# Kernel tuning notes

Measured on AMD Instinct MI355X. Metric: run time of the kernel, lower is better.

## Reference

```python
import jax, jax.numpy as jnp
import numpy as np

B, S, D = 2, 1024, 1024
L, E, F = 2, 8, 2048


def setup_inputs() -> dict:
    key = jax.random.key(0)
    kx, kp, k1, k2 = jax.random.split(key, 4)
    x = jax.random.normal(kx, (B, S, D), dtype=jnp.float32)
    # prototypes scaled so dot products are O(1), keeping softmax well-behaved
    protos = jax.random.normal(kp, (L, E, D), dtype=jnp.float32) / np.sqrt(D)
    W1 = jax.random.normal(k1, (L, E, D, F), dtype=jnp.float32) * 0.02
    W2 = jax.random.normal(k2, (L, E, F, D), dtype=jnp.float32) * 0.02
    return {"x": x, "protos": protos, "W1": W1, "W2": W2, "k": 2}


def _route(x, protos_l, k):
    # expert_mapping: abs(dot(prototype, input)) per expert, keep top-k, rest -> -inf, softmax
    scores = jnp.abs(jnp.einsum("bsd,ed->bse", x, protos_l))  # [B,S,E]
    topv, _ = jax.lax.top_k(scores, k)
    thresh = topv[..., -1:]  # k-th largest per token
    masked = jnp.where(scores >= thresh, scores, -jnp.inf)
    return jax.nn.softmax(masked, axis=-1)  # [B,S,E]


def reference(x, protos, W1, W2, k):
    n_layers = protos.shape[0]
    for l in range(n_layers):  # fixed small layer loop
        w = _route(x, protos[l], k)  # [B,S,E]
        h = jax.nn.relu(jnp.einsum("bsd,edf->bsef", x, W1[l]))  # [B,S,E,F]
        y = jnp.einsum("bsef,efd,bse->bsd", h, W2[l], w)  # weighted expert mix
        x = x + y
    return x
```

## Files before the change

kernel.cpp:

```cpp
#include <hip/hip_runtime.h>
#include <hip/hip_bf16.h>
#include <cstdint>

#define T_TOKENS 2048
#define DDIM 1024
#define FDIM 2048
#define NEXP 8
#define NLAYER 2
#define BMPAD 64
#define RMAX 4608

#define ATILE_EL 2048
#define BTILE_EL 4096

typedef unsigned short u16;
typedef short bf16x8 __attribute__((ext_vector_type(8)));
typedef u16 u16x8 __attribute__((ext_vector_type(8)));
typedef u16 u16x4v __attribute__((ext_vector_type(4)));
typedef float f32x4 __attribute__((ext_vector_type(4)));

__device__ __forceinline__ u16 bf16_rn(float f) {
  unsigned u = __builtin_bit_cast(unsigned, f);
  u += 0x7fffu + ((u >> 16) & 1u);
  return (u16)(u >> 16);
}
__device__ __forceinline__ float bf16_f(u16 h) {
  unsigned u = ((unsigned)h) << 16;
  return __builtin_bit_cast(float, u);
}

__device__ __forceinline__ void gl16(const void* g, void* l) {
  __builtin_amdgcn_global_load_lds((const __attribute__((address_space(1))) void*)g,
                                   (__attribute__((address_space(3))) void*)l, 16, 0, 0);
}

__global__ __launch_bounds__(256) void route_kernel(
    const float* __restrict__ x, const float* __restrict__ protos,
    int* __restrict__ eid, float* __restrict__ wgt) {
  const int t = blockIdx.x;
  const int tid = threadIdx.x;
  const float* xr = x + (size_t)t * DDIM;
  __shared__ float red[NEXP][256];
  float acc[NEXP];
#pragma unroll
  for (int e = 0; e < NEXP; ++e) acc[e] = 0.f;
  for (int d = tid; d < DDIM; d += 256) {
    float xv = xr[d];
#pragma unroll
    for (int e = 0; e < NEXP; ++e) acc[e] += xv * protos[e * DDIM + d];
  }
#pragma unroll
  for (int e = 0; e < NEXP; ++e) red[e][tid] = acc[e];
  __syncthreads();
  for (int s = 128; s > 0; s >>= 1) {
    if (tid < s) {
#pragma unroll
      for (int e = 0; e < NEXP; ++e) red[e][tid] += red[e][tid + s];
    }
    __syncthreads();
  }
  if (tid == 0) {
    float m1 = -1.f, m2 = -1.f;
    int i1 = 0, i2 = 0;
#pragma unroll
    for (int e = 0; e < NEXP; ++e) {
      float s = fabsf(red[e][0]);
      if (s > m1) { m2 = m1; i2 = i1; m1 = s; i1 = e; }
      else if (s > m2) { m2 = s; i2 = e; }
    }
    float e2 = __expf(m2 - m1);
    float z = 1.f + e2;
    eid[t * 2] = i1;
    eid[t * 2 + 1] = i2;
    wgt[t * 2] = 1.f / z;
    wgt[t * 2 + 1] = e2 / z;
  }
}

__global__ __launch_bounds__(256) void compact_kernel(
    const int* __restrict__ eid, int* __restrict__ cnt, int* __restrict__ offp,
    int* __restrict__ row2token, int* __restrict__ pos) {
  __shared__ int lcnt[NEXP][256];
  __shared__ int s_off[NEXP], s_tot[NEXP];
  const int tid = threadIdx.x;
  const int base = tid * 16;

  int my[16];
#pragma unroll
  for (int i = 0; i < 4; ++i)
    *(int4*)&my[i * 4] = *(const int4*)(eid + base + i * 4);

#pragma unroll
  for (int e = 0; e < NEXP; ++e) {
    int c = 0;
#pragma unroll
    for (int i = 0; i < 16; ++i) c += (my[i] == e) ? 1 : 0;
    lcnt[e][tid] = c;
  }

  for (int r = tid; r < RMAX; r += 256) row2token[r] = -1;
  __syncthreads();

  if (tid < NEXP) {
    int run = 0;
    for (int i = 0; i < 256; ++i) {
      int v = lcnt[tid][i];
      lcnt[tid][i] = run;
      run += v;
    }
    s_tot[tid] = run;
  }
  __syncthreads();
  if (tid == 0) {
    int o = 0;
    for (int e = 0; e < NEXP; ++e) {
      s_off[e] = o;
      o += (s_tot[e] + BMPAD - 1) & ~(BMPAD - 1);
    }
  }
  __syncthreads();

  int myoff[NEXP];
#pragma unroll
  for (int e = 0; e < NEXP; ++e) myoff[e] = s_off[e] + lcnt[e][tid];
#pragma unroll
  for (int i = 0; i < 16; ++i) {
    int r = 0;
#pragma unroll
    for (int e = 0; e < NEXP; ++e) r = (my[i] == e) ? myoff[e] : r;
    row2token[r] = (base + i) >> 1;
    pos[base + i] = r;
#pragma unroll
    for (int e = 0; e < NEXP; ++e) myoff[e] += (my[i] == e) ? 1 : 0;
  }

  if (tid < NEXP) {
    cnt[tid] = s_tot[tid];
    offp[tid] = s_off[tid];
  }
}

__global__ __launch_bounds__(256) void gather_kernel(
    const float* __restrict__ x, const int* __restrict__ row2token,
    u16* __restrict__ Ahi, u16* __restrict__ Alo) {
  const int r = blockIdx.x;
  const int t = row2token[r];
  const int c = threadIdx.x * 4;
  float4 v = make_float4(0.f, 0.f, 0.f, 0.f);
  if (t >= 0) v = *(const float4*)(x + (size_t)t * DDIM + c);
  float vv[4] = {v.x, v.y, v.z, v.w};
  u16x4v hi, lo;
#pragma unroll
  for (int i = 0; i < 4; ++i) {
    u16 h = bf16_rn(vv[i]);
    hi[i] = h;
    lo[i] = bf16_rn(vv[i] - bf16_f(h));
  }
  const size_t el = ((size_t)(r >> 6) * (DDIM >> 5) + (c >> 5)) * ATILE_EL +
                    (size_t)(((c >> 3) & 3) * 64 + (r & 63)) * 8 + (c & 7);
  *(u16x4v*)(Ahi + el) = hi;
  *(u16x4v*)(Alo + el) = lo;
}

template <bool LO>
__global__ __launch_bounds__(256) void wconv_kernel(
    const float* __restrict__ W, u16* __restrict__ Hi, u16* __restrict__ Lo,
    int K, int N) {
  const int e = blockIdx.z, nb = blockIdx.x, kb = blockIdx.y;
  const float* Wp = W + ((size_t)e * K + (size_t)kb * 32) * N + nb * 128;
  __shared__ float tile[32][129];
  const int t = threadIdx.x;
#pragma unroll
  for (int i = 0; i < 4; ++i) {
    const int f4 = i * 256 + t;
    const int kr = f4 >> 5;
    const int c4 = (f4 & 31) * 4;
    float4 v = *(const float4*)(Wp + (size_t)kr * N + c4);
    *(float4*)&tile[kr][c4] = v;
  }
  __syncthreads();
  const size_t tb = (((size_t)e * (N >> 7) + nb) * (K >> 5) + kb) * BTILE_EL;
#pragma unroll
  for (int j = 0; j < 2; ++j) {
    const int cid = j * 256 + t;
    const int n = cid & 127, ksel = cid >> 7;
    u16x8 hv, lv;
#pragma unroll
    for (int i = 0; i < 8; ++i) {
      float f = tile[ksel * 8 + i][n];
      u16 h = bf16_rn(f);
      hv[i] = h;
      if (LO) lv[i] = bf16_rn(f - bf16_f(h));
    }
    *(u16x8*)(Hi + tb + (size_t)cid * 8) = hv;
    if (LO) *(u16x8*)(Lo + tb + (size_t)cid * 8) = lv;
  }
}

template <bool RELU, bool SPLIT, int OUTMODE>
__global__ __launch_bounds__(256, SPLIT ? 3 : 4) void gemm_mfma(
    const u16* __restrict__ Ahi, const u16* __restrict__ Alo,
    const u16* __restrict__ Bhi, const u16* __restrict__ Blo,
    u16* __restrict__ OutHi, u16* __restrict__ OutLo, float* __restrict__ OutF,
    const int* __restrict__ cnt, const int* __restrict__ offp, int K, int N) {
  const int e = blockIdx.z;
  const int cp = (cnt[e] + 63) & ~63;
  if ((int)(blockIdx.y * 64) >= cp) return;
  const int row0 = offp[e] + blockIdx.y * 64;
  const int n0 = blockIdx.x * 128;
  const int nkb = K >> 5;

  constexpr int BUF_EL = SPLIT ? 12288 : 6144;
  __shared__ u16 lds[2 * BUF_EL];

  const int tid = threadIdx.x;
  const int lane = tid & 63;
  const int wid = tid >> 6;
  const int wr = wid >> 1, wc = wid & 1;
  const int lr = lane & 15, kg = lane >> 4;
  const int lo16 = lane << 4;

  f32x4 acc[2][4];
#pragma unroll
  for (int i = 0; i < 2; ++i)
#pragma unroll
    for (int j = 0; j < 4; ++j)
#pragma unroll
      for (int r = 0; r < 4; ++r) acc[i][j][r] = 0.f;

  const size_t abase = (size_t)(row0 >> 6) * nkb * ATILE_EL;
  const size_t bbase = ((size_t)e * (N >> 7) + (n0 >> 7)) * nkb * BTILE_EL;

  auto STAGE = [&](int kb, int b) {
    char* d = (char*)(lds + b * BUF_EL);
    const char* gah = (const char*)(Ahi + abase + (size_t)kb * ATILE_EL);
    const char* gbh = (const char*)(Bhi + bbase + (size_t)kb * BTILE_EL);
    if constexpr (SPLIT) {
      const char* gal = (const char*)(Alo + abase + (size_t)kb * ATILE_EL);
      const char* gbl = (const char*)(Blo + bbase + (size_t)kb * BTILE_EL);
      if (wid == 0) {
#pragma unroll
        for (int i = 0; i < 4; ++i) gl16(gah + i * 1024 + lo16, d + i * 1024);
#pragma unroll
        for (int i = 0; i < 4; ++i) gl16(gal + i * 1024 + lo16, d + 4096 + i * 1024);
      } else if (wid == 1) {
#pragma unroll
        for (int i = 0; i < 8; ++i) gl16(gbh + i * 1024 + lo16, d + 8192 + i * 1024);
      } else if (wid == 2) {
#pragma unroll
        for (int i = 0; i < 8; ++i) gl16(gbl + i * 1024 + lo16, d + 16384 + i * 1024);
      }
    } else {
      if (wid == 0) {
#pragma unroll
        for (int i = 0; i < 4; ++i) gl16(gah + i * 1024 + lo16, d + i * 1024);
      } else if (wid == 1) {
#pragma unroll
        for (int i = 0; i < 4; ++i) gl16(gbh + i * 1024 + lo16, d + 4096 + i * 1024);
      } else if (wid == 2) {
#pragma unroll
        for (int i = 0; i < 4; ++i) gl16(gbh + 4096 + i * 1024 + lo16, d + 8192 + i * 1024);
      }
    }
  };

  STAGE(0, 0);
  __syncthreads();

  int cur = 0;
  for (int kb = 0; kb < nkb; ++kb) {
    if (kb + 1 < nkb) STAGE(kb + 1, cur ^ 1);

    const u16* buf = lds + cur * BUF_EL;
    const u16* AsH = buf;
    const u16* BsH = buf + (SPLIT ? 4096 : 2048);
    bf16x8 ah0 = *(const bf16x8*)&AsH[(kg * 64 + wr * 32 + lr) * 8];
    bf16x8 ah1 = *(const bf16x8*)&AsH[(kg * 64 + wr * 32 + 16 + lr) * 8];
    bf16x8 bh[4];
#pragma unroll
    for (int j = 0; j < 4; ++j)
      bh[j] = *(const bf16x8*)&BsH[(kg * 128 + wc * 64 + j * 16 + lr) * 8];
#pragma unroll
    for (int j = 0; j < 4; ++j) {
      acc[0][j] = __builtin_amdgcn_mfma_f32_16x16x32_bf16(ah0, bh[j], acc[0][j], 0, 0, 0);
      acc[1][j] = __builtin_amdgcn_mfma_f32_16x16x32_bf16(ah1, bh[j], acc[1][j], 0, 0, 0);
    }
    if constexpr (SPLIT) {
      const u16* AsL = buf + 2048;
      const u16* BsL = buf + 8192;
      bf16x8 al0 = *(const bf16x8*)&AsL[(kg * 64 + wr * 32 + lr) * 8];
      bf16x8 al1 = *(const bf16x8*)&AsL[(kg * 64 + wr * 32 + 16 + lr) * 8];
#pragma unroll
      for (int j = 0; j < 4; ++j) {
        bf16x8 bl = *(const bf16x8*)&BsL[(kg * 128 + wc * 64 + j * 16 + lr) * 8];
        acc[0][j] = __builtin_amdgcn_mfma_f32_16x16x32_bf16(ah0, bl, acc[0][j], 0, 0, 0);
        acc[1][j] = __builtin_amdgcn_mfma_f32_16x16x32_bf16(ah1, bl, acc[1][j], 0, 0, 0);
        acc[0][j] = __builtin_amdgcn_mfma_f32_16x16x32_bf16(al0, bh[j], acc[0][j], 0, 0, 0);
        acc[1][j] = __builtin_amdgcn_mfma_f32_16x16x32_bf16(al1, bh[j], acc[1][j], 0, 0, 0);
      }
    }
    __syncthreads();
    cur ^= 1;
  }

  const int nkbO = N >> 5;
#pragma unroll
  for (int i = 0; i < 2; ++i) {
#pragma unroll
    for (int j = 0; j < 4; ++j) {
      const int Cj = n0 + wc * 64 + j * 16 + lr;
      f32x4 v = acc[i][j];
#pragma unroll
      for (int r = 0; r < 4; ++r) {
        const int R = row0 + wr * 32 + i * 16 + kg * 4 + r;
        float f = v[r];
        if (RELU) f = fmaxf(f, 0.f);
        if constexpr (OUTMODE == 0) {
          OutF[(size_t)R * N + Cj] = f;
        } else {
          const size_t el = ((size_t)(R >> 6) * nkbO + (Cj >> 5)) * ATILE_EL +
                            (size_t)(((Cj >> 3) & 3) * 64 + (R & 63)) * 8 + (Cj & 7);
          u16 h = bf16_rn(f);
          OutHi[el] = h;
          if constexpr (OUTMODE == 1) OutLo[el] = bf16_rn(f - bf16_f(h));
        }
      }
    }
  }
}

__global__ __launch_bounds__(256) void apply_kernel(
    const float* __restrict__ ytmp, const int* __restrict__ pos,
    const float* __restrict__ wgt, float* __restrict__ x) {
  const int t = blockIdx.x;
  const int c = threadIdx.x * 4;
  const int p0 = pos[t * 2], p1 = pos[t * 2 + 1];
  const float w0 = wgt[t * 2], w1 = wgt[t * 2 + 1];
  float4 xa = *(float4*)(x + (size_t)t * DDIM + c);
  const float4 y0 = *(const float4*)(ytmp + (size_t)p0 * DDIM + c);
  const float4 y1 = *(const float4*)(ytmp + (size_t)p1 * DDIM + c);
  xa.x += w0 * y0.x + w1 * y1.x;
  xa.y += w0 * y0.y + w1 * y1.y;
  xa.z += w0 * y0.z + w1 * y1.z;
  xa.w += w0 * y0.w + w1 * y1.w;
  *(float4*)(x + (size_t)t * DDIM + c) = xa;
}

extern "C" void kernel_launch(void* const* d_in, const int* in_sizes, int n_in,
                              void* d_out, int out_size, void* d_ws, size_t ws_size,
                              hipStream_t stream) {
  const float* x = (const float*)d_in[0];
  const float* protos = (const float*)d_in[1];
  const float* W1 = (const float*)d_in[2];
  const float* W2 = (const float*)d_in[3];
  float* xcur = (float*)d_out;

  u16* W_hi = (u16*)d_ws;
  u16* W_lo = W_hi + (size_t)NEXP * DDIM * FDIM;
  u16* Ag_hi = W_lo + (size_t)NEXP * DDIM * FDIM;
  u16* Ag_lo = Ag_hi + (size_t)RMAX * DDIM;
  u16* h_hi = Ag_lo + (size_t)RMAX * DDIM;
  u16* h_lo = h_hi + (size_t)RMAX * FDIM;
  float* ytmp = (float*)(h_lo + (size_t)RMAX * FDIM);
  float* wgt = ytmp + (size_t)RMAX * DDIM;
  int* eid = (int*)(wgt + T_TOKENS * 2);
  int* pos = eid + T_TOKENS * 2;
  int* cnt = pos + T_TOKENS * 2;
  int* offp = cnt + NEXP;
  int* row2token = offp + NEXP;

  hipMemcpyAsync(xcur, x, (size_t)T_TOKENS * DDIM * sizeof(float),
                 hipMemcpyDeviceToDevice, stream);

  for (int l = 0; l < NLAYER; ++l) {
    route_kernel<<<T_TOKENS, 256, 0, stream>>>(
        xcur, protos + (size_t)l * NEXP * DDIM, eid, wgt);
    compact_kernel<<<1, 256, 0, stream>>>(eid, cnt, offp, row2token, pos);
    gather_kernel<<<RMAX, 256, 0, stream>>>(xcur, row2token, Ag_hi, Ag_lo);
    const float* W1l = W1 + (size_t)l * NEXP * DDIM * FDIM;
    const float* W2l = W2 + (size_t)l * NEXP * FDIM * DDIM;
    if (l == 0) {
      wconv_kernel<true><<<dim3(FDIM / 128, DDIM / 32, NEXP), 256, 0, stream>>>(
          W1l, W_hi, W_lo, DDIM, FDIM);
      gemm_mfma<true, true, 1><<<dim3(FDIM / 128, RMAX / 64, NEXP), 256, 0, stream>>>(
          Ag_hi, Ag_lo, W_hi, W_lo, h_hi, h_lo, nullptr, cnt, offp, DDIM, FDIM);
      wconv_kernel<true><<<dim3(DDIM / 128, FDIM / 32, NEXP), 256, 0, stream>>>(
          W2l, W_hi, W_lo, FDIM, DDIM);
      gemm_mfma<false, true, 0><<<dim3(DDIM / 128, RMAX / 64, NEXP), 256, 0, stream>>>(
          h_hi, h_lo, W_hi, W_lo, nullptr, nullptr, ytmp, cnt, offp, FDIM, DDIM);
    } else {
      wconv_kernel<false><<<dim3(FDIM / 128, DDIM / 32, NEXP), 256, 0, stream>>>(
          W1l, W_hi, nullptr, DDIM, FDIM);
      gemm_mfma<true, false, 2><<<dim3(FDIM / 128, RMAX / 64, NEXP), 256, 0, stream>>>(
          Ag_hi, nullptr, W_hi, nullptr, h_hi, nullptr, nullptr, cnt, offp, DDIM, FDIM);
      wconv_kernel<false><<<dim3(DDIM / 128, FDIM / 32, NEXP), 256, 0, stream>>>(
          W2l, W_hi, nullptr, FDIM, DDIM);
      gemm_mfma<false, false, 0><<<dim3(DDIM / 128, RMAX / 64, NEXP), 256, 0, stream>>>(
          h_hi, nullptr, W_hi, nullptr, nullptr, nullptr, ytmp, cnt, offp, FDIM, DDIM);
    }
    apply_kernel<<<T_TOKENS, 256, 0, stream>>>(ytmp, pos, wgt, xcur);
  }
}
```

Baseline: 381.1 us.

## Enlarge GEMM M-tile to 128 rows and split-K the down projection

The expert GEMM tile grows from 64x128 to 128x128, with each wave computing a 64x64 sub-tile (4x4 MFMAs), which doubles operand reuse per LDS load and halves the B-tile traffic per output. The second GEMM (K=2048) is split into two K halves written to separate partial buffers, which the apply kernel sums, restoring grid parallelism lost by the larger tile. Padding rows past each expert's count are masked on store, and buffers are enlarged (RALLOC) to cover 128-row overrun. Costs are higher register and LDS use (occupancy lowered to 2 for the split path) and extra partial-buffer traffic.

After: 392.9 us. 1.03x slower.

```diff
diff --git a/kernel.cpp b/kernel.cpp
--- a/kernel.cpp
+++ b/kernel.cpp
@@ -9,6 +9,7 @@
 #define NLAYER 2
 #define BMPAD 64
 #define RMAX 4608
+#define RALLOC 4736
 
 #define ATILE_EL 2048
 #define BTILE_EL 4096
@@ -197,20 +198,24 @@
   }
 }
 
-template <bool RELU, bool SPLIT, int OUTMODE>
-__global__ __launch_bounds__(256, SPLIT ? 3 : 4) void gemm_mfma(
+template <bool RELU, bool SPLIT, int OUTMODE, int SKF>
+__global__ __launch_bounds__(256, SPLIT ? 2 : 4) void gemm_mfma(
     const u16* __restrict__ Ahi, const u16* __restrict__ Alo,
     const u16* __restrict__ Bhi, const u16* __restrict__ Blo,
     u16* __restrict__ OutHi, u16* __restrict__ OutLo, float* __restrict__ OutF,
     const int* __restrict__ cnt, const int* __restrict__ offp, int K, int N) {
-  const int e = blockIdx.z;
+  const int z = blockIdx.z;
+  const int e = z / SKF, sk = z % SKF;
   const int cp = (cnt[e] + 63) & ~63;
-  if ((int)(blockIdx.y * 64) >= cp) return;
-  const int row0 = offp[e] + blockIdx.y * 64;
+  if ((int)(blockIdx.y * 128) >= cp) return;
+  const int row0 = offp[e] + blockIdx.y * 128;
+  const int rend = offp[e] + cp;
   const int n0 = blockIdx.x * 128;
   const int nkb = K >> 5;
-
-  constexpr int BUF_EL = SPLIT ? 12288 : 6144;
+  const int kbN = nkb / SKF;
+  const int kb0 = sk * kbN;
+
+  constexpr int BUF_EL = SPLIT ? 16384 : 8192;
   __shared__ u16 lds[2 * BUF_EL];
 
   const int tid = threadIdx.x;
@@ -220,84 +225,99 @@
   const int lr = lane & 15, kg = lane >> 4;
   const int lo16 = lane << 4;
 
-  f32x4 acc[2][4];
-#pragma unroll
-  for (int i = 0; i < 2; ++i)
+  f32x4 acc[4][4];
+#pragma unroll
+  for (int i = 0; i < 4; ++i)
 #pragma unroll
     for (int j = 0; j < 4; ++j)
 #pragma unroll
       for (int r = 0; r < 4; ++r) acc[i][j][r] = 0.f;
 
-  const size_t abase = (size_t)(row0 >> 6) * nkb * ATILE_EL;
-  const size_t bbase = ((size_t)e * (N >> 7) + (n0 >> 7)) * nkb * BTILE_EL;
+  const int at0 = row0 >> 6;
+  const size_t bbase = ((size_t)e * (N >> 7) + (n0 >> 7)) * nkb;
 
   auto STAGE = [&](int kb, int b) {
     char* d = (char*)(lds + b * BUF_EL);
-    const char* gah = (const char*)(Ahi + abase + (size_t)kb * ATILE_EL);
-    const char* gbh = (const char*)(Bhi + bbase + (size_t)kb * BTILE_EL);
     if constexpr (SPLIT) {
-      const char* gal = (const char*)(Alo + abase + (size_t)kb * ATILE_EL);
-      const char* gbl = (const char*)(Blo + bbase + (size_t)kb * BTILE_EL);
       if (wid == 0) {
 #pragma unroll
-        for (int i = 0; i < 4; ++i) gl16(gah + i * 1024 + lo16, d + i * 1024);
-#pragma unroll
-        for (int i = 0; i < 4; ++i) gl16(gal + i * 1024 + lo16, d + 4096 + i * 1024);
+        for (int t = 0; t < 2; ++t) {
+          const char* g = (const char*)(Ahi + ((size_t)(at0 + t) * nkb + kb) * ATILE_EL);
+#pragma unroll
+          for (int i = 0; i < 4; ++i) gl16(g + i * 1024 + lo16, d + t * 4096 + i * 1024);
+        }
       } else if (wid == 1) {
 #pragma unroll
-        for (int i = 0; i < 8; ++i) gl16(gbh + i * 1024 + lo16, d + 8192 + i * 1024);
+        for (int t = 0; t < 2; ++t) {
+          const char* g = (const char*)(Alo + ((size_t)(at0 + t) * nkb + kb) * ATILE_EL);
+#pragma unroll
+          for (int i = 0; i < 4; ++i) gl16(g + i * 1024 + lo16, d + 8192 + t * 4096 + i * 1024);
+        }
       } else if (wid == 2) {
-#pragma unroll
-        for (int i = 0; i < 8; ++i) gl16(gbl + i * 1024 + lo16, d + 16384 + i * 1024);
+        const char* g = (const char*)(Bhi + (bbase + kb) * BTILE_EL);
+#pragma unroll
+        for (int i = 0; i < 8; ++i) gl16(g + i * 1024 + lo16, d + 16384 + i * 1024);
+      } else {
+        const char* g = (const char*)(Blo + (bbase + kb) * BTILE_EL);
+#pragma unroll
+        for (int i = 0; i < 8; ++i) gl16(g + i * 1024 + lo16, d + 24576 + i * 1024);
       }
     } else {
-      if (wid == 0) {
-#pragma unroll
-        for (int i = 0; i < 4; ++i) gl16(gah + i * 1024 + lo16, d + i * 1024);
-      } else if (wid == 1) {
-#pragma unroll
-        for (int i = 0; i < 4; ++i) gl16(gbh + i * 1024 + lo16, d + 4096 + i * 1024);
-      } else if (wid == 2) {
-#pragma unroll
-        for (int i = 0; i < 4; ++i) gl16(gbh + 4096 + i * 1024 + lo16, d + 8192 + i * 1024);
+      if (wid < 2) {
+        const char* g = (const char*)(Ahi + ((size_t)(at0 + wid) * nkb + kb) * ATILE_EL);
+#pragma unroll
+        for (int i = 0; i < 4; ++i) gl16(g + i * 1024 + lo16, d + wid * 4096 + i * 1024);
+      } else {
+        const char* g = (const char*)(Bhi + (bbase + kb) * BTILE_EL) + (wid - 2) * 4096;
+#pragma unroll
+        for (int i = 0; i < 4; ++i) gl16(g + i * 1024 + lo16, d + 8192 + (wid - 2) * 4096 + i * 1024);
       }
     }
   };
 
-  STAGE(0, 0);
+  STAGE(kb0, 0);
   __syncthreads();
 
   int cur = 0;
-  for (int kb = 0; kb < nkb; ++kb) {
-    if (kb + 1 < nkb) STAGE(kb + 1, cur ^ 1);
+  for (int kb = kb0; kb < kb0 + kbN; ++kb) {
+    if (kb + 1 < kb0 + kbN) STAGE(kb + 1, cur ^ 1);
 
     const u16* buf = lds + cur * BUF_EL;
-    const u16* AsH = buf;
-    const u16* BsH = buf + (SPLIT ? 4096 : 2048);
-    bf16x8 ah0 = *(const bf16x8*)&AsH[(kg * 64 + wr * 32 + lr) * 8];
-    bf16x8 ah1 = *(const bf16x8*)&AsH[(kg * 64 + wr * 32 + 16 + lr) * 8];
-    bf16x8 bh[4];
-#pragma unroll
-    for (int j = 0; j < 4; ++j)
-      bh[j] = *(const bf16x8*)&BsH[(kg * 128 + wc * 64 + j * 16 + lr) * 8];
-#pragma unroll
-    for (int j = 0; j < 4; ++j) {
-      acc[0][j] = __builtin_amdgcn_mfma_f32_16x16x32_bf16(ah0, bh[j], acc[0][j], 0, 0, 0);
-      acc[1][j] = __builtin_amdgcn_mfma_f32_16x16x32_bf16(ah1, bh[j], acc[1][j], 0, 0, 0);
-    }
+    const u16* AsH = buf + wr * 2048;
+    const u16* BsH = buf + (SPLIT ? 8192 : 4096);
+    const int arow = (kg * 64 + lr) * 8;
+    const int bcol = (kg * 128 + wc * 64 + lr) * 8;
+
+    bf16x8 ah[4], bh[4];
+#pragma unroll
+    for (int i = 0; i < 4; ++i) ah[i] = *(const bf16x8*)&AsH[arow + i * 128];
+#pragma unroll
+    for (int j = 0; j < 4; ++j) bh[j] = *(const bf16x8*)&BsH[bcol + j * 128];
+#pragma unroll
+    for (int i = 0; i < 4; ++i)
+#pragma unroll
+      for (int j = 0; j < 4; ++j)
+        acc[i][j] = __builtin_amdgcn_mfma_f32_16x16x32_bf16(ah[i], bh[j], acc[i][j], 0, 0, 0);
+
     if constexpr (SPLIT) {
-      const u16* AsL = buf + 2048;
-      const u16* BsL = buf + 8192;
-      bf16x8 al0 = *(const bf16x8*)&AsL[(kg * 64 + wr * 32 + lr) * 8];
-      bf16x8 al1 = *(const bf16x8*)&AsL[(kg * 64 + wr * 32 + 16 + lr) * 8];
-#pragma unroll
-      for (int j = 0; j < 4; ++j) {
-        bf16x8 bl = *(const bf16x8*)&BsL[(kg * 128 + wc * 64 + j * 16 + lr) * 8];
-        acc[0][j] = __builtin_amdgcn_mfma_f32_16x16x32_bf16(ah0, bl, acc[0][j], 0, 0, 0);
-        acc[1][j] = __builtin_amdgcn_mfma_f32_16x16x32_bf16(ah1, bl, acc[1][j], 0, 0, 0);
-        acc[0][j] = __builtin_amdgcn_mfma_f32_16x16x32_bf16(al0, bh[j], acc[0][j], 0, 0, 0);
-        acc[1][j] = __builtin_amdgcn_mfma_f32_16x16x32_bf16(al1, bh[j], acc[1][j], 0, 0, 0);
-      }
+      const u16* AsL = buf + 4096 + wr * 2048;
+      const u16* BsL = buf + 12288;
+      bf16x8 bl[4];
+#pragma unroll
+      for (int j = 0; j < 4; ++j) bl[j] = *(const bf16x8*)&BsL[bcol + j * 128];
+#pragma unroll
+      for (int i = 0; i < 4; ++i)
+#pragma unroll
+        for (int j = 0; j < 4; ++j)
+          acc[i][j] = __builtin_amdgcn_mfma_f32_16x16x32_bf16(ah[i], bl[j], acc[i][j], 0, 0, 0);
+      bf16x8 al[4];
+#pragma unroll
+      for (int i = 0; i < 4; ++i) al[i] = *(const bf16x8*)&AsL[arow + i * 128];
+#pragma unroll
+      for (int i = 0; i < 4; ++i)
+#pragma unroll
+        for (int j = 0; j < 4; ++j)
+          acc[i][j] = __builtin_amdgcn_mfma_f32_16x16x32_bf16(al[i], bh[j], acc[i][j], 0, 0, 0);
     }
     __syncthreads();
     cur ^= 1;
@@ -305,18 +325,19 @@
 
   const int nkbO = N >> 5;
 #pragma unroll
-  for (int i = 0; i < 2; ++i) {
+  for (int i = 0; i < 4; ++i) {
 #pragma unroll
     for (int j = 0; j < 4; ++j) {
       const int Cj = n0 + wc * 64 + j * 16 + lr;
       f32x4 v = acc[i][j];
 #pragma unroll
       for (int r = 0; r < 4; ++r) {
-        const int R = row0 + wr * 32 + i * 16 + kg * 4 + r;
+        const int R = row0 + wr * 64 + i * 16 + kg * 4 + r;
+        if (R >= rend) continue;
         float f = v[r];
         if (RELU) f = fmaxf(f, 0.f);
         if constexpr (OUTMODE == 0) {
-          OutF[(size_t)R * N + Cj] = f;
+          OutF[((size_t)sk * RALLOC + R) * N + Cj] = f;
         } else {
           const size_t el = ((size_t)(R >> 6) * nkbO + (Cj >> 5)) * ATILE_EL +
                             (size_t)(((Cj >> 3) & 3) * 64 + (R & 63)) * 8 + (Cj & 7);
@@ -330,19 +351,23 @@
 }
 
 __global__ __launch_bounds__(256) void apply_kernel(
-    const float* __restrict__ ytmp, const int* __restrict__ pos,
+    const float* __restrict__ part, const int* __restrict__ pos,
     const float* __restrict__ wgt, float* __restrict__ x) {
   const int t = blockIdx.x;
   const int c = threadIdx.x * 4;
   const int p0 = pos[t * 2], p1 = pos[t * 2 + 1];
   const float w0 = wgt[t * 2], w1 = wgt[t * 2 + 1];
+  const float* P0 = part;
+  const float* P1 = part + (size_t)RALLOC * DDIM;
   float4 xa = *(float4*)(x + (size_t)t * DDIM + c);
-  const float4 y0 = *(const float4*)(ytmp + (size_t)p0 * DDIM + c);
-  const float4 y1 = *(const float4*)(ytmp + (size_t)p1 * DDIM + c);
-  xa.x += w0 * y0.x + w1 * y1.x;
-  xa.y += w0 * y0.y + w1 * y1.y;
-  xa.z += w0 * y0.z + w1 * y1.z;
-  xa.w += w0 * y0.w + w1 * y1.w;
+  const float4 a0 = *(const float4*)(P0 + (size_t)p0 * DDIM + c);
+  const float4 b0 = *(const float4*)(P1 + (size_t)p0 * DDIM + c);
+  const float4 a1 = *(const float4*)(P0 + (size_t)p1 * DDIM + c);
+  const float4 b1 = *(const float4*)(P1 + (size_t)p1 * DDIM + c);
+  xa.x += w0 * (a0.x + b0.x) + w1 * (a1.x + b1.x);
+  xa.y += w0 * (a0.y + b0.y) + w1 * (a1.y + b1.y);
+  xa.z += w0 * (a0.z + b0.z) + w1 * (a1.z + b1.z);
+  xa.w += w0 * (a0.w + b0.w) + w1 * (a1.w + b1.w);
   *(float4*)(x + (size_t)t * DDIM + c) = xa;
 }
 
@@ -358,11 +383,11 @@
   u16* W_hi = (u16*)d_ws;
   u16* W_lo = W_hi + (size_t)NEXP * DDIM * FDIM;
   u16* Ag_hi = W_lo + (size_t)NEXP * DDIM * FDIM;
-  u16* Ag_lo = Ag_hi + (size_t)RMAX * DDIM;
-  u16* h_hi = Ag_lo + (size_t)RMAX * DDIM;
-  u16* h_lo = h_hi + (size_t)RMAX * FDIM;
-  float* ytmp = (float*)(h_lo + (size_t)RMAX * FDIM);
-  float* wgt = ytmp + (size_t)RMAX * DDIM;
+  u16* Ag_lo = Ag_hi + (size_t)RALLOC * DDIM;
+  u16* h_hi = Ag_lo + (size_t)RALLOC * DDIM;
+  u16* h_lo = h_hi + (size_t)RALLOC * FDIM;
+  float* part = (float*)(h_lo + (size_t)RALLOC * FDIM);
+  float* wgt = part + (size_t)2 * RALLOC * DDIM;
   int* eid = (int*)(wgt + T_TOKENS * 2);
   int* pos = eid + T_TOKENS * 2;
   int* cnt = pos + T_TOKENS * 2;
@@ -382,22 +407,22 @@
     if (l == 0) {
       wconv_kernel<true><<<dim3(FDIM / 128, DDIM / 32, NEXP), 256, 0, stream>>>(
           W1l, W_hi, W_lo, DDIM, FDIM);
-      gemm_mfma<true, true, 1><<<dim3(FDIM / 128, RMAX / 64, NEXP), 256, 0, stream>>>(
+      gemm_mfma<true, true, 1, 1><<<dim3(FDIM / 128, RMAX / 128, NEXP), 256, 0, stream>>>(
           Ag_hi, Ag_lo, W_hi, W_lo, h_hi, h_lo, nullptr, cnt, offp, DDIM, FDIM);
       wconv_kernel<true><<<dim3(DDIM / 128, FDIM / 32, NEXP), 256, 0, stream>>>(
           W2l, W_hi, W_lo, FDIM, DDIM);
-      gemm_mfma<false, true, 0><<<dim3(DDIM / 128, RMAX / 64, NEXP), 256, 0, stream>>>(
-          h_hi, h_lo, W_hi, W_lo, nullptr, nullptr, ytmp, cnt, offp, FDIM, DDIM);
+      gemm_mfma<false, true, 0, 2><<<dim3(DDIM / 128, RMAX / 128, NEXP * 2), 256, 0, stream>>>(
+          h_hi, h_lo, W_hi, W_lo, nullptr, nullptr, part, cnt, offp, FDIM, DDIM);
     } else {
       wconv_kernel<false><<<dim3(FDIM / 128, DDIM / 32, NEXP), 256, 0, stream>>>(
           W1l, W_hi, nullptr, DDIM, FDIM);
-      gemm_mfma<true, false, 2><<<dim3(FDIM / 128, RMAX / 64, NEXP), 256, 0, stream>>>(
+      gemm_mfma<true, false, 2, 1><<<dim3(FDIM / 128, RMAX / 128, NEXP), 256, 0, stream>>>(
           Ag_hi, nullptr, W_hi, nullptr, h_hi, nullptr, nullptr, cnt, offp, DDIM, FDIM);
       wconv_kernel<false><<<dim3(DDIM / 128, FDIM / 32, NEXP), 256, 0, stream>>>(
           W2l, W_hi, nullptr, FDIM, DDIM);
-      gemm_mfma<false, false, 0><<<dim3(DDIM / 128, RMAX / 64, NEXP), 256, 0, stream>>>(
-          h_hi, nullptr, W_hi, nullptr, nullptr, nullptr, ytmp, cnt, offp, FDIM, DDIM);
-    }
-    apply_kernel<<<T_TOKENS, 256, 0, stream>>>(ytmp, pos, wgt, xcur);
-  }
-}
+      gemm_mfma<false, false, 0, 2><<<dim3(DDIM / 128, RMAX / 128, NEXP * 2), 256, 0, stream>>>(
+          h_hi, nullptr, W_hi, nullptr, nullptr, nullptr, part, cnt, offp, FDIM, DDIM);
+    }
+    apply_kernel<<<T_TOKENS, 256, 0, stream>>>(part, pos, wgt, xcur);
+  }
+}
```
